# Kernel optimization log

Hardware: AMD Instinct MI355X
Metric: run time of the kernel (lower is better)

## Reference

```python
import jax, jax.numpy as jnp
import numpy as np

C = 512  # channels

def _maxpool2x2(x):
    # x: [B,H,W,C] -> [B,H/2,W/2,C]
    B, H, W, Cc = x.shape
    return x.reshape(B, H // 2, 2, W // 2, 2, Cc).max(axis=(2, 4))

def setup_inputs() -> dict:
    key = jax.random.key(0)
    ks = jax.random.split(key, 6)
    x = jax.random.normal(ks[0], (16, 64, 64, C), dtype=jnp.float32)
    # 1x1 conv kernels stored as [C_in, C_out]; spectral norm treated as identity
    # on the (already-normalized) effective weights.
    s = lambda k, i, o: jax.random.normal(k, (i, o), dtype=jnp.float32) / np.sqrt(i)
    W_theta = s(ks[1], C, C // 8)
    W_phi = s(ks[2], C, C // 8)
    W_g = s(ks[3], C, C // 2)
    W_o = s(ks[4], C // 2, C)
    gamma = jnp.float32(0.7)  # nonzero so the attention path matters
    return {"x": x, "W_theta": W_theta, "W_phi": W_phi, "W_g": W_g,
            "W_o": W_o, "gamma": gamma}

def reference(x, W_theta, W_phi, W_g, W_o, gamma):
    B, H, W, Cc = x.shape
    S = H * W            # query length
    Sk = S // 4          # key/value length after 2x2 maxpool
    theta = jnp.einsum('bhwc,cd->bhwd', x, W_theta)              # [B,H,W,C/8]
    phi = _maxpool2x2(jnp.einsum('bhwc,cd->bhwd', x, W_phi))     # [B,H/2,W/2,C/8]
    g = _maxpool2x2(jnp.einsum('bhwc,cd->bhwd', x, W_g))         # [B,H/2,W/2,C/2]
    theta = theta.reshape(B, S, Cc // 8)
    phi = phi.reshape(B, Sk, Cc // 8)
    g = g.reshape(B, Sk, Cc // 2)
    # scores [B,S,Sk]; SAGAN omits the 1/sqrt(d_k) scaling
    beta = jax.nn.softmax(jnp.einsum('bqd,bkd->bqk', theta, phi), axis=-1)
    tmp = jnp.einsum('bqk,bkv->bqv', beta, g).reshape(B, H, W, Cc // 2)
    o = jnp.einsum('bhwv,vc->bhwc', tmp, W_o)
    return gamma * o + x
```

## Files before the change

kernel.cpp:

```cpp
#include <hip/hip_runtime.h>

typedef __attribute__((ext_vector_type(8))) short bf16x8;
typedef __attribute__((ext_vector_type(4))) float f32x4;
typedef unsigned short u16;
typedef unsigned int u32;

#define MFMA __builtin_amdgcn_mfma_f32_16x16x32_bf16

static __device__ __forceinline__ float b2f(u16 u) {
    u32 x = ((u32)u) << 16;
    return __builtin_bit_cast(float, x);
}
static __device__ __forceinline__ u16 f2b(float f) {
    u32 u = __builtin_bit_cast(u32, f);
    u32 r = (u + 0x7fffu + ((u >> 16) & 1u)) >> 16;
    return (u16)r;
}
static __device__ __forceinline__ void async16(const u16* g, u16* l) {
    __builtin_amdgcn_global_load_lds(
        (const __attribute__((address_space(1))) u32*)g,
        (__attribute__((address_space(3))) u32*)l, 16, 0, 0);
}

__global__ __launch_bounds__(256) void xcast(const float* __restrict__ x, u16* __restrict__ xb) {
    size_t i = ((size_t)blockIdx.x * 256 + threadIdx.x) * 8;
    f32x4 f0 = *(const f32x4*)(x + i);
    f32x4 f1 = *(const f32x4*)(x + i + 4);
    bf16x8 v;
    v[0] = (short)f2b(f0[0]); v[1] = (short)f2b(f0[1]);
    v[2] = (short)f2b(f0[2]); v[3] = (short)f2b(f0[3]);
    v[4] = (short)f2b(f1[0]); v[5] = (short)f2b(f1[1]);
    v[6] = (short)f2b(f1[2]); v[7] = (short)f2b(f1[3]);
    *(bf16x8*)(xb + i) = v;
}

__global__ void pack_w(const float* __restrict__ Wt, const float* __restrict__ Wp,
                       const float* __restrict__ Wg, const float* __restrict__ Wo,
                       u16* __restrict__ WcatT, u16* __restrict__ WoT) {
    int t = blockIdx.x * 256 + threadIdx.x;
    const int n1 = 384 * 512;
    if (t < n1) {
        int n = t >> 9, k = t & 511;
        float v;
        if (n < 64)       v = Wt[k * 64 + n];
        else if (n < 128) v = Wp[k * 64 + (n - 64)];
        else              v = Wg[k * 256 + (n - 128)];
        WcatT[t] = f2b(v);
    } else {
        int j = t - n1;
        if (j < 512 * 256) {
            int n = j >> 8, k = j & 255;
            WoT[j] = f2b(Wo[k * 512 + n]);
        }
    }
}

template <int K>
static __device__ __forceinline__ void gemm_core(const u16* __restrict__ A,
                                                 const u16* __restrict__ Bt,
                                                 int m0, int n0, int lda, int ldb,
                                                 f32x4 acc[4][4], u16* S) {
    const int t = threadIdx.x;
    const int w = t >> 6, li = t & 15, quad = (t >> 4) & 3;
    const int wm = (w & 1) << 6, wn = (w >> 1) << 6;
#pragma unroll
    for (int mi = 0; mi < 4; mi++)
#pragma unroll
        for (int ni = 0; ni < 4; ni++) acc[mi][ni] = (f32x4)0.0f;
    const u16* ag = A + (size_t)(m0 + (t >> 2)) * lda + ((t & 3) << 3);
    const u16* bg = Bt + (size_t)(n0 + (t >> 2)) * ldb + ((t & 3) << 3);
    const int ws = w * 512;
    async16(ag, S + ws);
    async16(ag + (size_t)64 * lda, S + ws + 2048);
    async16(bg, S + 4096 + ws);
    async16(bg + (size_t)64 * ldb, S + 4096 + ws + 2048);
    __syncthreads();
    int cur = 0;
#pragma unroll
    for (int k0 = 0; k0 < K; k0 += 32) {
        if (k0 + 32 < K) {
            u16* nS = S + (cur ^ 1) * 8192;
            async16(ag + k0 + 32, nS + ws);
            async16(ag + k0 + 32 + (size_t)64 * lda, nS + ws + 2048);
            async16(bg + k0 + 32, nS + 4096 + ws);
            async16(bg + k0 + 32 + (size_t)64 * ldb, nS + 4096 + ws + 2048);
        }
        const u16* As = S + cur * 8192;
        const u16* Bs = As + 4096;
        bf16x8 af[4], bfr[4];
#pragma unroll
        for (int mi = 0; mi < 4; mi++)
            af[mi] = *(const bf16x8*)(As + (wm + mi * 16 + li) * 32 + quad * 8);
#pragma unroll
        for (int ni = 0; ni < 4; ni++)
            bfr[ni] = *(const bf16x8*)(Bs + (wn + ni * 16 + li) * 32 + quad * 8);
#pragma unroll
        for (int mi = 0; mi < 4; mi++)
#pragma unroll
            for (int ni = 0; ni < 4; ni++)
                acc[mi][ni] = MFMA(af[mi], bfr[ni], acc[mi][ni], 0, 0, 0);
        __syncthreads();
        cur ^= 1;
    }
}

static __device__ __forceinline__ void epi_bf16(const f32x4 acc[4][4], u16* ebuf,
                                                u16* __restrict__ outp, int ld,
                                                int row0, int col0) {
    const int t = threadIdx.x;
    const int li = t & 15, quad = (t >> 4) & 3;
    const int rr = (t & 63) >> 3, cc = (t & 7) * 8;
#pragma unroll
    for (int h = 0; h < 2; h++) {
#pragma unroll
        for (int m2 = 0; m2 < 2; m2++)
#pragma unroll
            for (int ni = 0; ni < 4; ni++)
#pragma unroll
                for (int r = 0; r < 4; r++)
                    ebuf[(m2 * 16 + quad * 4 + r) * 72 + ni * 16 + li] =
                        f2b(acc[h * 2 + m2][ni][r]);
#pragma unroll
        for (int j = 0; j < 4; j++) {
            int row = j * 8 + rr;
            bf16x8 v = *(const bf16x8*)(ebuf + row * 72 + cc);
            *(bf16x8*)(outp + (size_t)(row0 + h * 32 + row) * ld + col0 + cc) = v;
        }
    }
}

__global__ __launch_bounds__(256) void proj_gemm(const u16* __restrict__ xb,
                                                 const u16* __restrict__ WcatT,
                                                 u16* __restrict__ theta,
                                                 u16* __restrict__ ppg) {
    __shared__ __attribute__((aligned(16))) u16 sbuf[16384];
    int bid = blockIdx.x;
    int sbid = (bid & 7) * 192 + (bid >> 3);
    int bm = sbid / 3, bn = sbid % 3;
    f32x4 acc[4][4];
    gemm_core<512>(xb, WcatT, bm * 128, bn * 128, 512, 512, acc, sbuf);
    const int w = threadIdx.x >> 6;
    u16* ebuf = sbuf + w * 2304;
    int row0 = bm * 128 + (w & 1) * 64;
    int gcol = bn * 128 + (w >> 1) * 64;
    if (gcol < 64) epi_bf16(acc, ebuf, theta, 64, row0, 0);
    else           epi_bf16(acc, ebuf, ppg, 320, row0, gcol - 64);
}

__global__ void pool_phi(const u16* __restrict__ ppg, u16* __restrict__ phi) {
    int t = blockIdx.x * 256 + threadIdx.x;
    int c = t & 63;
    int pos = (t >> 6) & 1023;
    int b = t >> 16;
    int h2 = pos >> 5, w2 = pos & 31;
    size_t base = ((size_t)(b << 12) + h2 * 128 + w2 * 2) * 320 + c;
    float v0 = b2f(ppg[base]), v1 = b2f(ppg[base + 320]);
    float v2 = b2f(ppg[base + 320 * 64]), v3 = b2f(ppg[base + 320 * 65]);
    float m = fmaxf(fmaxf(v0, v1), fmaxf(v2, v3));
    phi[((size_t)(b << 10) + pos) * 64 + c] = f2b(m);
}

__global__ void pool_gt(const u16* __restrict__ ppg, u16* __restrict__ gT) {
    __shared__ float tile[64][65];
    int bid = blockIdx.x;
    int b = bid >> 6;
    int rem = bid & 63;
    int c0 = (rem >> 4) * 64;
    int pos0 = (rem & 15) * 64;
    int t = threadIdx.x;
#pragma unroll
    for (int i = 0; i < 16; i++) {
        int o = t + i * 256;
        int cl = o & 63, pl = o >> 6;
        int pos = pos0 + pl;
        int h2 = pos >> 5, w2 = pos & 31;
        size_t base = ((size_t)(b << 12) + h2 * 128 + w2 * 2) * 320 + 64 + c0 + cl;
        float v0 = b2f(ppg[base]), v1 = b2f(ppg[base + 320]);
        float v2 = b2f(ppg[base + 320 * 64]), v3 = b2f(ppg[base + 320 * 65]);
        tile[pl][cl] = fmaxf(fmaxf(v0, v1), fmaxf(v2, v3));
    }
    __syncthreads();
    int cl = t >> 2, ch = t & 3;
    u16 valbuf[16] __attribute__((aligned(16)));
#pragma unroll
    for (int j = 0; j < 16; j++) valbuf[j] = f2b(tile[ch * 16 + j][cl]);
    u16* dst = gT + ((size_t)b * 256 + c0 + cl) * 1024 + pos0 + ch * 16;
    *(uint4*)(dst) = *(const uint4*)(valbuf);
    *(uint4*)(dst + 8) = *(const uint4*)(valbuf + 8);
}

__global__ __launch_bounds__(256, 2) void attn_fused(const u16* __restrict__ theta,
                                                     const u16* __restrict__ phi,
                                                     const u16* __restrict__ gT,
                                                     u16* __restrict__ tmp) {
    __shared__ __attribute__((aligned(16))) u16 lds[28672];
    u16* stgP = lds;
    u16* stgG = lds + 4096;
    u16* pbuf = lds + 20480;

    int bid = blockIdx.x;
    int swz = (bid & 7) * 64 + (bid >> 3);
    int b = swz >> 5;
    int q0 = (swz & 31) << 7;
    const int t = threadIdx.x;
    const int w = t >> 6, li = t & 15, quad = (t >> 4) & 3;

    const u16* thp = theta + (((size_t)(b << 12) + q0 + w * 32 + li) << 6) + quad * 8;
    bf16x8 tq[2][2];
    tq[0][0] = *(const bf16x8*)thp;
    tq[0][1] = *(const bf16x8*)(thp + 32);
    tq[1][0] = *(const bf16x8*)(thp + (16 << 6));
    tq[1][1] = *(const bf16x8*)(thp + (16 << 6) + 32);

    const int srow = t >> 3;
    const int sc = (t & 7) ^ (srow & 7);
    const u16* phisrc = phi + ((size_t)(b << 10) + srow) * 64 + sc * 8;
    const u16* gsrc = gT + ((size_t)(b << 8) + srow) * 1024 + sc * 8;
    u16* pbq[2] = {pbuf + (w * 2 + 0) * 1024, pbuf + (w * 2 + 1) * 1024};

    f32x4 o[2][16];
#pragma unroll
    for (int qg = 0; qg < 2; qg++)
#pragma unroll
        for (int ni = 0; ni < 16; ni++) o[qg][ni] = (f32x4)0.0f;
    float m[2] = {-3.0e38f, -3.0e38f}, sum[2] = {0.0f, 0.0f};

    for (int kc = 0; kc < 16; kc++) {
        __syncthreads();
        async16(phisrc + (size_t)(kc * 64) * 64, stgP + w * 512);
        async16(phisrc + (size_t)(kc * 64 + 32) * 64, stgP + 2048 + w * 512);
#pragma unroll
        for (int j = 0; j < 8; j++)
            async16(gsrc + (size_t)(j * 32) * 1024 + kc * 64, stgG + j * 2048 + w * 512);
        __syncthreads();

        f32x4 sacc[2][4];
#pragma unroll
        for (int qg = 0; qg < 2; qg++)
#pragma unroll
            for (int nf = 0; nf < 4; nf++) sacc[qg][nf] = (f32x4)0.0f;
#pragma unroll
        for (int nf = 0; nf < 4; nf++) {
            int row = nf * 16 + li;
            int p0 = quad ^ (li & 7);
            int p1 = (4 + quad) ^ (li & 7);
            bf16x8 f0 = *(const bf16x8*)(stgP + row * 64 + p0 * 8);
            bf16x8 f1 = *(const bf16x8*)(stgP + row * 64 + p1 * 8);
            sacc[0][nf] = MFMA(f0, tq[0][0], sacc[0][nf], 0, 0, 0);
            sacc[0][nf] = MFMA(f1, tq[0][1], sacc[0][nf], 0, 0, 0);
            sacc[1][nf] = MFMA(f0, tq[1][0], sacc[1][nf], 0, 0, 0);
            sacc[1][nf] = MFMA(f1, tq[1][1], sacc[1][nf], 0, 0, 0);
        }

#pragma unroll
        for (int qg = 0; qg < 2; qg++) {
            float mc = sacc[qg][0][0];
#pragma unroll
            for (int nf = 0; nf < 4; nf++)
#pragma unroll
                for (int r = 0; r < 4; r++) mc = fmaxf(mc, sacc[qg][nf][r]);
            mc = fmaxf(mc, __shfl_xor(mc, 16, 64));
            mc = fmaxf(mc, __shfl_xor(mc, 32, 64));
            if (!__all(mc <= m[qg] + 8.0f)) {
                float nm = fmaxf(m[qg], mc);
                float f = __expf(m[qg] - nm);
                sum[qg] *= f;
#pragma unroll
                for (int ni = 0; ni < 16; ni++)
#pragma unroll
                    for (int r = 0; r < 4; r++) o[qg][ni][r] *= f;
                m[qg] = nm;
            }
            float p[16];
            float s = 0.0f;
#pragma unroll
            for (int nf = 0; nf < 4; nf++)
#pragma unroll
                for (int r = 0; r < 4; r++) {
                    float e = __expf(sacc[qg][nf][r] - m[qg]);
                    p[nf * 4 + r] = e;
                    s += e;
                }
            s += __shfl_xor(s, 16, 64);
            s += __shfl_xor(s, 32, 64);
            sum[qg] += s;

            u16* pb = pbq[qg];
#pragma unroll
            for (int nf = 0; nf < 4; nf++) {
                int cc = nf * 2 + (quad >> 1);
                int pos = cc ^ (li & 7);
                u32* dst = (u32*)(pb + li * 64 + pos * 8 + (quad & 1) * 4);
                dst[0] = (u32)f2b(p[nf * 4 + 0]) | ((u32)f2b(p[nf * 4 + 1]) << 16);
                dst[1] = (u32)f2b(p[nf * 4 + 2]) | ((u32)f2b(p[nf * 4 + 3]) << 16);
            }
        }

#pragma unroll
        for (int w2 = 0; w2 < 2; w2++) {
            int pos8 = ((w2 * 4 + quad) ^ (li & 7)) * 8;
            bf16x8 pf0 = *(const bf16x8*)(pbq[0] + li * 64 + pos8);
            bf16x8 pf1 = *(const bf16x8*)(pbq[1] + li * 64 + pos8);
#pragma unroll
            for (int ni = 0; ni < 16; ni++) {
                bf16x8 gf = *(const bf16x8*)(stgG + (ni * 16 + li) * 64 + pos8);
                o[0][ni] = MFMA(gf, pf0, o[0][ni], 0, 0, 0);
                o[1][ni] = MFMA(gf, pf1, o[1][ni], 0, 0, 0);
            }
        }
    }

    float inv[2] = {1.0f / sum[0], 1.0f / sum[1]};
#pragma unroll
    for (int qg = 0; qg < 2; qg++)
#pragma unroll
        for (int ni = 0; ni < 16; ni++)
#pragma unroll
            for (int r = 0; r < 4; r++) o[qg][ni][r] *= inv[qg];

    __syncthreads();
    u16* eb = lds + w * 4224;
    const int lane = t & 63;
#pragma unroll
    for (int qg = 0; qg < 2; qg++) {
#pragma unroll
        for (int ni = 0; ni < 16; ni++) {
            u32* d = (u32*)(eb + li * 264 + ni * 16 + quad * 4);
            d[0] = (u32)f2b(o[qg][ni][0]) | ((u32)f2b(o[qg][ni][1]) << 16);
            d[1] = (u32)f2b(o[qg][ni][2]) | ((u32)f2b(o[qg][ni][3]) << 16);
        }
#pragma unroll
        for (int pss = 0; pss < 8; pss++) {
            int row = pss * 2 + (lane >> 5);
            bf16x8 v = *(const bf16x8*)(eb + row * 264 + (lane & 31) * 8);
            *(bf16x8*)(tmp + ((size_t)(b << 12) + q0 + w * 32 + qg * 16 + row) * 256 +
                       (lane & 31) * 8) = v;
        }
    }
}

__global__ __launch_bounds__(256) void out_gemm(const u16* __restrict__ tmp,
                                                const u16* __restrict__ WoT,
                                                const float* __restrict__ x,
                                                const float* __restrict__ gamma_p,
                                                float* __restrict__ out) {
    __shared__ __attribute__((aligned(16))) u16 sbuf[16384];
    int bid = blockIdx.x;
    int sbid = (bid & 7) * 256 + (bid >> 3);
    int bm = sbid >> 2, bn = sbid & 3;
    f32x4 acc[4][4];
    gemm_core<256>(tmp, WoT, bm * 128, bn * 128, 256, 256, acc, sbuf);
    float gamma = gamma_p[0];
    const int t = threadIdx.x;
    const int w = t >> 6, li = t & 15, quad = (t >> 4) & 3;
    int row0 = bm * 128 + (w & 1) * 64;
    int col0 = bn * 128 + (w >> 1) * 64;
    float* fb = (float*)sbuf + w * 1088;
    const int lane = t & 63;
    const int rhi = lane >> 4, cl = (lane & 15) * 4;
#pragma unroll
    for (int mi = 0; mi < 4; mi++) {
        f32x4 xv[4];
#pragma unroll
        for (int j = 0; j < 4; j++) {
            size_t go = (size_t)(row0 + mi * 16 + j * 4 + rhi) * 512 + col0 + cl;
            xv[j] = *(const f32x4*)(x + go);
        }
#pragma unroll
        for (int ni = 0; ni < 4; ni++)
#pragma unroll
            for (int r = 0; r < 4; r++)
                fb[(quad * 4 + r) * 68 + ni * 16 + li] = acc[mi][ni][r];
#pragma unroll
        for (int j = 0; j < 4; j++) {
            f32x4 v = *(const f32x4*)(fb + (j * 4 + rhi) * 68 + cl);
#pragma unroll
            for (int e = 0; e < 4; e++) v[e] = gamma * v[e] + xv[j][e];
            size_t go = (size_t)(row0 + mi * 16 + j * 4 + rhi) * 512 + col0 + cl;
            *(f32x4*)(out + go) = v;
        }
    }
}

extern "C" void kernel_launch(void* const* d_in, const int* in_sizes, int n_in,
                              void* d_out, int out_size, void* d_ws, size_t ws_size,
                              hipStream_t stream) {
    (void)in_sizes; (void)n_in; (void)out_size; (void)ws_size;
    const float* x  = (const float*)d_in[0];
    const float* Wt = (const float*)d_in[1];
    const float* Wp = (const float*)d_in[2];
    const float* Wg = (const float*)d_in[3];
    const float* Wo = (const float*)d_in[4];
    const float* gm = (const float*)d_in[5];
    float* out = (float*)d_out;

    char* ws = (char*)d_ws;
    size_t off = 0;
    u16* WcatT = (u16*)(ws + off); off += (size_t)384 * 512 * 2;
    u16* WoT   = (u16*)(ws + off); off += (size_t)512 * 256 * 2;
    u16* xb    = (u16*)(ws + off); off += (size_t)65536 * 512 * 2;
    u16* theta = (u16*)(ws + off); off += (size_t)65536 * 64 * 2;
    u16* ppg   = (u16*)(ws + off); off += (size_t)65536 * 320 * 2;
    u16* phi = xb;
    u16* gT  = xb + (size_t)16 * 1024 * 64;
    u16* tmp = ppg;

    pack_w<<<1280, 256, 0, stream>>>(Wt, Wp, Wg, Wo, WcatT, WoT);
    xcast<<<16384, 256, 0, stream>>>(x, xb);
    proj_gemm<<<1536, 256, 0, stream>>>(xb, WcatT, theta, ppg);
    pool_phi<<<4096, 256, 0, stream>>>(ppg, phi);
    pool_gt<<<1024, 256, 0, stream>>>(ppg, gT);
    attn_fused<<<512, 256, 0, stream>>>(theta, phi, gT, tmp);
    out_gemm<<<2048, 256, 0, stream>>>(tmp, WoT, x, gm, out);
}
```

Before: 389.7 us.

## Fuse fp32-to-bf16 cast and 2x2 maxpool into projection GEMM

The projection GEMM now reads fp32 x directly, converting to bf16 in registers before staging A tiles in LDS, which removes the separate xcast kernel and its bf16 copy of x. The epilogue stages the tile in a swizzled LDS buffer and performs the 2x2 max-pool in-block, writing theta, pooled phi and transposed pooled g directly. This drops the pool_phi and pool_gt kernels and the full-resolution ppg intermediate. In exchange, the GEMM loads twice as many bytes for A through plain global loads rather than async LDS copies, and the pooling relies on 128-row tiles mapping to two image rows.

```diff
diff --git a/kernel.cpp b/kernel.cpp
--- a/kernel.cpp
+++ b/kernel.cpp
@@ -20,18 +20,6 @@
     __builtin_amdgcn_global_load_lds(
         (const __attribute__((address_space(1))) u32*)g,
         (__attribute__((address_space(3))) u32*)l, 16, 0, 0);
-}
-
-__global__ __launch_bounds__(256) void xcast(const float* __restrict__ x, u16* __restrict__ xb) {
-    size_t i = ((size_t)blockIdx.x * 256 + threadIdx.x) * 8;
-    f32x4 f0 = *(const f32x4*)(x + i);
-    f32x4 f1 = *(const f32x4*)(x + i + 4);
-    bf16x8 v;
-    v[0] = (short)f2b(f0[0]); v[1] = (short)f2b(f0[1]);
-    v[2] = (short)f2b(f0[2]); v[3] = (short)f2b(f0[3]);
-    v[4] = (short)f2b(f1[0]); v[5] = (short)f2b(f1[1]);
-    v[6] = (short)f2b(f1[2]); v[7] = (short)f2b(f1[3]);
-    *(bf16x8*)(xb + i) = v;
 }
 
 __global__ void pack_w(const float* __restrict__ Wt, const float* __restrict__ Wp,
@@ -104,89 +92,158 @@
     }
 }
 
-static __device__ __forceinline__ void epi_bf16(const f32x4 acc[4][4], u16* ebuf,
-                                                u16* __restrict__ outp, int ld,
-                                                int row0, int col0) {
+template <int K>
+static __device__ __forceinline__ void gemm_core_f32(const float* __restrict__ A,
+                                                     const u16* __restrict__ Bt,
+                                                     int m0, int n0, int lda, int ldb,
+                                                     f32x4 acc[4][4], u16* S) {
     const int t = threadIdx.x;
-    const int li = t & 15, quad = (t >> 4) & 3;
-    const int rr = (t & 63) >> 3, cc = (t & 7) * 8;
-#pragma unroll
-    for (int h = 0; h < 2; h++) {
-#pragma unroll
-        for (int m2 = 0; m2 < 2; m2++)
+    const int w = t >> 6, li = t & 15, quad = (t >> 4) & 3;
+    const int wm = (w & 1) << 6, wn = (w >> 1) << 6;
+#pragma unroll
+    for (int mi = 0; mi < 4; mi++)
+#pragma unroll
+        for (int ni = 0; ni < 4; ni++) acc[mi][ni] = (f32x4)0.0f;
+    const float* ag = A + (size_t)(m0 + (t >> 2)) * lda + ((t & 3) << 3);
+    const u16* bg = Bt + (size_t)(n0 + (t >> 2)) * ldb + ((t & 3) << 3);
+    const int ws = w * 512;
+    {
+        f32x4 a00 = *(const f32x4*)(ag);
+        f32x4 a01 = *(const f32x4*)(ag + 4);
+        f32x4 a10 = *(const f32x4*)(ag + (size_t)64 * lda);
+        f32x4 a11 = *(const f32x4*)(ag + (size_t)64 * lda + 4);
+        async16(bg, S + 4096 + ws);
+        async16(bg + (size_t)64 * ldb, S + 4096 + ws + 2048);
+        bf16x8 v0, v1;
+#pragma unroll
+        for (int e = 0; e < 4; e++) {
+            v0[e] = (short)f2b(a00[e]); v0[4 + e] = (short)f2b(a01[e]);
+            v1[e] = (short)f2b(a10[e]); v1[4 + e] = (short)f2b(a11[e]);
+        }
+        *(bf16x8*)(S + t * 8) = v0;
+        *(bf16x8*)(S + 2048 + t * 8) = v1;
+    }
+    __syncthreads();
+    int cur = 0;
+#pragma unroll
+    for (int k0 = 0; k0 < K; k0 += 32) {
+        f32x4 a00, a01, a10, a11;
+        if (k0 + 32 < K) {
+            a00 = *(const f32x4*)(ag + k0 + 32);
+            a01 = *(const f32x4*)(ag + k0 + 36);
+            a10 = *(const f32x4*)(ag + k0 + 32 + (size_t)64 * lda);
+            a11 = *(const f32x4*)(ag + k0 + 36 + (size_t)64 * lda);
+            u16* nS = S + (cur ^ 1) * 8192;
+            async16(bg + k0 + 32, nS + 4096 + ws);
+            async16(bg + k0 + 32 + (size_t)64 * ldb, nS + 4096 + ws + 2048);
+        }
+        const u16* As = S + cur * 8192;
+        const u16* Bs = As + 4096;
+        bf16x8 af[4], bfr[4];
+#pragma unroll
+        for (int mi = 0; mi < 4; mi++)
+            af[mi] = *(const bf16x8*)(As + (wm + mi * 16 + li) * 32 + quad * 8);
+#pragma unroll
+        for (int ni = 0; ni < 4; ni++)
+            bfr[ni] = *(const bf16x8*)(Bs + (wn + ni * 16 + li) * 32 + quad * 8);
+#pragma unroll
+        for (int mi = 0; mi < 4; mi++)
 #pragma unroll
             for (int ni = 0; ni < 4; ni++)
-#pragma unroll
-                for (int r = 0; r < 4; r++)
-                    ebuf[(m2 * 16 + quad * 4 + r) * 72 + ni * 16 + li] =
-                        f2b(acc[h * 2 + m2][ni][r]);
-#pragma unroll
-        for (int j = 0; j < 4; j++) {
-            int row = j * 8 + rr;
-            bf16x8 v = *(const bf16x8*)(ebuf + row * 72 + cc);
-            *(bf16x8*)(outp + (size_t)(row0 + h * 32 + row) * ld + col0 + cc) = v;
-        }
-    }
-}
-
-__global__ __launch_bounds__(256) void proj_gemm(const u16* __restrict__ xb,
+                acc[mi][ni] = MFMA(af[mi], bfr[ni], acc[mi][ni], 0, 0, 0);
+        if (k0 + 32 < K) {
+            u16* nS = S + (cur ^ 1) * 8192;
+            bf16x8 v0, v1;
+#pragma unroll
+            for (int e = 0; e < 4; e++) {
+                v0[e] = (short)f2b(a00[e]); v0[4 + e] = (short)f2b(a01[e]);
+                v1[e] = (short)f2b(a10[e]); v1[4 + e] = (short)f2b(a11[e]);
+            }
+            *(bf16x8*)(nS + t * 8) = v0;
+            *(bf16x8*)(nS + 2048 + t * 8) = v1;
+        }
+        __syncthreads();
+        cur ^= 1;
+    }
+}
+
+__global__ __launch_bounds__(256) void proj_gemm(const float* __restrict__ x,
                                                  const u16* __restrict__ WcatT,
                                                  u16* __restrict__ theta,
-                                                 u16* __restrict__ ppg) {
-    __shared__ __attribute__((aligned(16))) u16 sbuf[16384];
+                                                 u16* __restrict__ phi,
+                                                 u16* __restrict__ gT) {
+    __shared__ __attribute__((aligned(16))) u16 S[16384];
     int bid = blockIdx.x;
     int sbid = (bid & 7) * 192 + (bid >> 3);
     int bm = sbid / 3, bn = sbid % 3;
+    int m0 = bm * 128;
     f32x4 acc[4][4];
-    gemm_core<512>(xb, WcatT, bm * 128, bn * 128, 512, 512, acc, sbuf);
-    const int w = threadIdx.x >> 6;
-    u16* ebuf = sbuf + w * 2304;
-    int row0 = bm * 128 + (w & 1) * 64;
-    int gcol = bn * 128 + (w >> 1) * 64;
-    if (gcol < 64) epi_bf16(acc, ebuf, theta, 64, row0, 0);
-    else           epi_bf16(acc, ebuf, ppg, 320, row0, gcol - 64);
-}
-
-__global__ void pool_phi(const u16* __restrict__ ppg, u16* __restrict__ phi) {
-    int t = blockIdx.x * 256 + threadIdx.x;
-    int c = t & 63;
-    int pos = (t >> 6) & 1023;
-    int b = t >> 16;
-    int h2 = pos >> 5, w2 = pos & 31;
-    size_t base = ((size_t)(b << 12) + h2 * 128 + w2 * 2) * 320 + c;
-    float v0 = b2f(ppg[base]), v1 = b2f(ppg[base + 320]);
-    float v2 = b2f(ppg[base + 320 * 64]), v3 = b2f(ppg[base + 320 * 65]);
-    float m = fmaxf(fmaxf(v0, v1), fmaxf(v2, v3));
-    phi[((size_t)(b << 10) + pos) * 64 + c] = f2b(m);
-}
-
-__global__ void pool_gt(const u16* __restrict__ ppg, u16* __restrict__ gT) {
-    __shared__ float tile[64][65];
-    int bid = blockIdx.x;
-    int b = bid >> 6;
-    int rem = bid & 63;
-    int c0 = (rem >> 4) * 64;
-    int pos0 = (rem & 15) * 64;
-    int t = threadIdx.x;
-#pragma unroll
-    for (int i = 0; i < 16; i++) {
-        int o = t + i * 256;
-        int cl = o & 63, pl = o >> 6;
-        int pos = pos0 + pl;
-        int h2 = pos >> 5, w2 = pos & 31;
-        size_t base = ((size_t)(b << 12) + h2 * 128 + w2 * 2) * 320 + 64 + c0 + cl;
-        float v0 = b2f(ppg[base]), v1 = b2f(ppg[base + 320]);
-        float v2 = b2f(ppg[base + 320 * 64]), v3 = b2f(ppg[base + 320 * 65]);
-        tile[pl][cl] = fmaxf(fmaxf(v0, v1), fmaxf(v2, v3));
-    }
+    gemm_core_f32<512>(x, WcatT, m0, bn * 128, 512, 512, acc, S);
+
+    const int t = threadIdx.x;
+    const int w = t >> 6, li = t & 15, quad = (t >> 4) & 3;
+    const int cbase = (w >> 1) << 6;
+    const int rbase = (w & 1) << 6;
+#pragma unroll
+    for (int mi = 0; mi < 4; mi++)
+#pragma unroll
+        for (int ni = 0; ni < 4; ni++) {
+            int c = cbase + ni * 16 + li;
+            int ch = c >> 3, ce = c & 7;
+#pragma unroll
+            for (int r = 0; r < 4; r++) {
+                int lr = rbase + mi * 16 + quad * 4 + r;
+                S[lr * 128 + ((ch ^ (lr & 7)) << 3) + ce] = f2b(acc[mi][ni][r]);
+            }
+        }
     __syncthreads();
-    int cl = t >> 2, ch = t & 3;
-    u16 valbuf[16] __attribute__((aligned(16)));
-#pragma unroll
-    for (int j = 0; j < 16; j++) valbuf[j] = f2b(tile[ch * 16 + j][cl]);
-    u16* dst = gT + ((size_t)b * 256 + c0 + cl) * 1024 + pos0 + ch * 16;
-    *(uint4*)(dst) = *(const uint4*)(valbuf);
-    *(uint4*)(dst + 8) = *(const uint4*)(valbuf + 8);
+
+    const int b = bm >> 5;
+    if (bn == 0) {
+        int lr = t >> 1;
+#pragma unroll
+        for (int k = 0; k < 4; k++) {
+            int ch = (t & 1) * 4 + k;
+            bf16x8 v = *(const bf16x8*)(S + lr * 128 + ((ch ^ (lr & 7)) << 3));
+            *(bf16x8*)(theta + (size_t)(m0 + lr) * 64 + (t & 1) * 32 + k * 8) = v;
+        }
+        int w2 = t >> 3;
+        int chp = 8 + (t & 7);
+        int r0 = 2 * w2, r1 = r0 + 1, r2 = r0 + 64, r3 = r0 + 65;
+        bf16x8 v0 = *(const bf16x8*)(S + r0 * 128 + ((chp ^ (r0 & 7)) << 3));
+        bf16x8 v1 = *(const bf16x8*)(S + r1 * 128 + ((chp ^ (r1 & 7)) << 3));
+        bf16x8 v2 = *(const bf16x8*)(S + r2 * 128 + ((chp ^ (r2 & 7)) << 3));
+        bf16x8 v3 = *(const bf16x8*)(S + r3 * 128 + ((chp ^ (r3 & 7)) << 3));
+        bf16x8 pv;
+#pragma unroll
+        for (int e = 0; e < 8; e++) {
+            float mv = fmaxf(fmaxf(b2f((u16)v0[e]), b2f((u16)v1[e])),
+                             fmaxf(b2f((u16)v2[e]), b2f((u16)v3[e])));
+            pv[e] = (short)f2b(mv);
+        }
+        int pos2 = (bm & 31) * 32 + w2;
+        *(bf16x8*)(phi + ((size_t)(b << 10) + pos2) * 64 + (t & 7) * 8) = pv;
+    } else {
+        const int c = t >> 1;
+        const int poff = (t & 1) * 16;
+        const int ch = c >> 3, ce = c & 7;
+        u16 vals[16] __attribute__((aligned(16)));
+#pragma unroll
+        for (int j = 0; j < 16; j++) {
+            int w2 = poff + j;
+            int r0 = 2 * w2, r1 = r0 + 1, r2 = r0 + 64, r3 = r0 + 65;
+            float m0v = b2f(S[r0 * 128 + ((ch ^ (r0 & 7)) << 3) + ce]);
+            float m1v = b2f(S[r1 * 128 + ((ch ^ (r1 & 7)) << 3) + ce]);
+            float m2v = b2f(S[r2 * 128 + ((ch ^ (r2 & 7)) << 3) + ce]);
+            float m3v = b2f(S[r3 * 128 + ((ch ^ (r3 & 7)) << 3) + ce]);
+            vals[j] = f2b(fmaxf(fmaxf(m0v, m1v), fmaxf(m2v, m3v)));
+        }
+        int cg = (bn - 1) * 128 + c;
+        int pos2b = (bm & 31) * 32 + poff;
+        u16* dst = gT + ((size_t)(b << 8) + cg) * 1024 + pos2b;
+        *(uint4*)dst = *(const uint4*)vals;
+        *(uint4*)(dst + 8) = *(const uint4*)(vals + 8);
+    }
 }
 
 __global__ __launch_bounds__(256, 2) void attn_fused(const u16* __restrict__ theta,
@@ -398,18 +455,13 @@
     size_t off = 0;
     u16* WcatT = (u16*)(ws + off); off += (size_t)384 * 512 * 2;
     u16* WoT   = (u16*)(ws + off); off += (size_t)512 * 256 * 2;
-    u16* xb    = (u16*)(ws + off); off += (size_t)65536 * 512 * 2;
+    u16* phi   = (u16*)(ws + off); off += (size_t)16 * 1024 * 64 * 2;
+    u16* gT    = (u16*)(ws + off); off += (size_t)16 * 256 * 1024 * 2;
     u16* theta = (u16*)(ws + off); off += (size_t)65536 * 64 * 2;
-    u16* ppg   = (u16*)(ws + off); off += (size_t)65536 * 320 * 2;
-    u16* phi = xb;
-    u16* gT  = xb + (size_t)16 * 1024 * 64;
-    u16* tmp = ppg;
+    u16* tmp   = (u16*)(ws + off); off += (size_t)65536 * 256 * 2;
 
     pack_w<<<1280, 256, 0, stream>>>(Wt, Wp, Wg, Wo, WcatT, WoT);
-    xcast<<<16384, 256, 0, stream>>>(x, xb);
-    proj_gemm<<<1536, 256, 0, stream>>>(xb, WcatT, theta, ppg);
-    pool_phi<<<4096, 256, 0, stream>>>(ppg, phi);
-    pool_gt<<<1024, 256, 0, stream>>>(ppg, gT);
+    proj_gemm<<<1536, 256, 0, stream>>>(x, WcatT, theta, phi, gT);
     attn_fused<<<512, 256, 0, stream>>>(theta, phi, gT, tmp);
     out_gemm<<<2048, 256, 0, stream>>>(tmp, WoT, x, gm, out);
 }
```

Measured after the change: 356.6 us. 8.5% less time.
